# Kernel optimization log

Measured on AMD Instinct MI355X. Metric: run time of the kernel, lower is better.

## Reference

```python
import jax, jax.numpy as jnp
import numpy as np

EPS = 1e-5

def setup_inputs() -> dict:
    key = jax.random.key(0)
    k1, k2, k3, k4, k5 = jax.random.split(key, 5)
    B, N, K, HW, C = 2, 128, 64, 65536, 134
    # class probabilities (rows need not be normalized for the matcher math)
    input_class_prob = jax.random.uniform(k1, (B, N, C), dtype=jnp.float32)
    # predicted mask probabilities in [0, 1]
    input_mask = jax.random.uniform(k2, (B, N, HW), dtype=jnp.float32)
    # binary ground-truth masks (stored as float32 for the reduction math)
    target_mask = (jax.random.uniform(k3, (B, K, HW)) > 0.7).astype(jnp.float32)
    target_class = jax.random.randint(k4, (B, K), 0, C, dtype=jnp.int64)
    target_sizes = jax.random.randint(k5, (B,), 1, K + 1, dtype=jnp.int64)
    return {
        "input_class_prob": input_class_prob,
        "input_mask": input_mask,
        "target_mask": target_mask,
        "target_class": target_class,
        "target_sizes": target_sizes,
    }


def reference(input_class_prob, input_mask, target_mask, target_class, target_sizes):
    """Similarity-matrix stage of HungarianMatcher.

    Returns sim: (B, N, K) = sim_class * sim_dice.
    The subsequent scipy linear_sum_assignment is CPU-only with
    data-dependent shapes and is excluded from the kernelizable math.
    """
    B, N, _ = input_class_prob.shape
    K = target_class.shape[-1]
    # sim_class[b, n, k] = input_class_prob[b, n, target_class[b, k]]
    idx = jnp.broadcast_to(target_class[:, None, :], (B, N, K))
    sim_class = jnp.take_along_axis(input_class_prob, idx, axis=-1)
    # dice similarity without materializing the (B, N, K, HW) broadcast:
    # intersections via GEMM, cardinalities via row/col sums + broadcast.
    intersections = jnp.einsum("bnp,bkp->bnk", input_mask, target_mask)
    cardinalities = input_mask.sum(-1)[:, :, None] + target_mask.sum(-1)[:, None, :]
    sim_dice = (2.0 * intersections + EPS) / (cardinalities + EPS)
    return sim_class * sim_dice
```

## Files before the change

kernel.cpp:

```cpp
#include <hip/hip_runtime.h>

#define HWX 65536
#define NQ 128
#define KT 64
#define CC 134
#define BB 2
#define NW 128
#define WIN 512
#define SUB 128
#define NSUB 4
#define EPSI 1e-5f

typedef __attribute__((ext_vector_type(4))) float f32x4;
typedef __attribute__((ext_vector_type(8))) short bf16x8;
typedef __attribute__((ext_vector_type(4))) unsigned int u32x4;

static __device__ __forceinline__ unsigned int cvtpk(float lo, float hi) {
  unsigned int r;
  asm("v_cvt_pk_bf16_f32 %0, %1, %2" : "=v"(r) : "v"(lo), "v"(hi));
  return r;
}

__global__ void hm_detect(const unsigned int* __restrict__ t,
                          unsigned int* __restrict__ flag) {
  unsigned int w = t[threadIdx.x * 2 + 1];
  unsigned long long any = __ballot(w != 0u);
  if (threadIdx.x == 0) *flag = (any != 0ull) ? 1u : 0u;
}

template <bool ATOMIC>
__global__ __launch_bounds__(512)
void hm_stage1(const float* __restrict__ in_mask, const float* __restrict__ tg_mask,
               float* __restrict__ Ipart, float* __restrict__ RSin,
               float* __restrict__ RStg) {
  const int w = blockIdx.x & (NW - 1);
  const int b = blockIdx.x >> 7;
  const int tid = threadIdx.x;
  const int lane = tid & 63;
  const int wv = tid >> 6;
  const int srow = tid >> 4;
  const int scolb = (tid & 15) * 16;
  const int l16 = lane & 15;
  const int lg = lane >> 4;

  __shared__ unsigned short lA[2][128 * 128];
  __shared__ unsigned short lB[2][64 * 128];

  const float* Ab = in_mask + (size_t)b * NQ * HWX + (size_t)w * WIN;
  const float* Bb = tg_mask + (size_t)b * KT * HWX + (size_t)w * WIN;

  f32x4 la[8], lb[4];
  f32x4 acc[4];
  #pragma unroll
  for (int i = 0; i < 4; ++i) acc[i] = f32x4{0.f, 0.f, 0.f, 0.f};
  float rsA[4] = {0.f, 0.f, 0.f, 0.f};
  float rsB[2] = {0.f, 0.f};

  auto ISSUE = [&](int t) {
    #pragma unroll
    for (int it = 0; it < 4; ++it) {
      const float* p = Ab + (size_t)(it * 32 + srow) * HWX + t * SUB + (tid & 15) * 8;
      la[it * 2]     = *(const f32x4*)p;
      la[it * 2 + 1] = *(const f32x4*)(p + 4);
    }
    #pragma unroll
    for (int it = 0; it < 2; ++it) {
      const float* p = Bb + (size_t)(it * 32 + srow) * HWX + t * SUB + (tid & 15) * 8;
      lb[it * 2]     = *(const f32x4*)p;
      lb[it * 2 + 1] = *(const f32x4*)(p + 4);
    }
  };

  auto CVTW = [&](int buf) {
    char* A8 = (char*)lA[buf];
    char* B8 = (char*)lB[buf];
    #pragma unroll
    for (int it = 0; it < 4; ++it) {
      f32x4 x = la[it * 2], y = la[it * 2 + 1];
      rsA[it] += (x.x + x.y) + (x.z + x.w) + (y.x + y.y) + (y.z + y.w);
      u32x4 v;
      v.x = cvtpk(x.x, x.y); v.y = cvtpk(x.z, x.w);
      v.z = cvtpk(y.x, y.y); v.w = cvtpk(y.z, y.w);
      const int row = it * 32 + srow;
      *(u32x4*)(A8 + ((row * 256 + scolb) ^ ((row & 7) << 4))) = v;
    }
    #pragma unroll
    for (int it = 0; it < 2; ++it) {
      f32x4 x = lb[it * 2], y = lb[it * 2 + 1];
      rsB[it] += (x.x + x.y) + (x.z + x.w) + (y.x + y.y) + (y.z + y.w);
      u32x4 v;
      v.x = cvtpk(x.x, x.y); v.y = cvtpk(x.z, x.w);
      v.z = cvtpk(y.x, y.y); v.w = cvtpk(y.z, y.w);
      const int row = it * 32 + srow;
      *(u32x4*)(B8 + ((row * 256 + scolb) ^ ((row & 7) << 4))) = v;
    }
  };

  auto COMP = [&](int buf) {
    const char* A8 = (const char*)lA[buf];
    const char* B8 = (const char*)lB[buf];
    const int arow = wv * 16 + l16;
    const int sw = (l16 & 7) << 4;
    #pragma unroll
    for (int s = 0; s < 4; ++s) {
      bf16x8 fa = *(const bf16x8*)(A8 + ((arow * 256 + s * 64 + lg * 16) ^ sw));
      #pragma unroll
      for (int cf = 0; cf < 4; ++cf) {
        const int brow = cf * 16 + l16;
        bf16x8 fb = *(const bf16x8*)(B8 + ((brow * 256 + s * 64 + lg * 16) ^ sw));
        acc[cf] = __builtin_amdgcn_mfma_f32_16x16x32_bf16(fa, fb, acc[cf], 0, 0, 0);
      }
    }
  };

  ISSUE(0);
  CVTW(0);
  __syncthreads();
  #pragma unroll
  for (int t = 0; t < NSUB; ++t) {
    if (t + 1 < NSUB) ISSUE(t + 1);
    COMP(t & 1);
    if (t + 1 < NSUB) {
      CVTW((t + 1) & 1);
      __syncthreads();
    }
  }

  #pragma unroll
  for (int cf = 0; cf < 4; ++cf) {
    #pragma unroll
    for (int j = 0; j < 4; ++j) {
      const int row = wv * 16 + lg * 4 + j;
      const int col = cf * 16 + l16;
      if (!ATOMIC)
        Ipart[((size_t)(b * NW + w) * NQ + row) * KT + col] = acc[cf][j];
      else
        atomicAdd(&Ipart[((size_t)b * NQ + row) * KT + col], acc[cf][j]);
    }
  }

  #pragma unroll
  for (int it = 0; it < 4; ++it) {
    float v = rsA[it];
    v += __shfl_xor(v, 1); v += __shfl_xor(v, 2);
    v += __shfl_xor(v, 4); v += __shfl_xor(v, 8);
    rsA[it] = v;
  }
  #pragma unroll
  for (int it = 0; it < 2; ++it) {
    float v = rsB[it];
    v += __shfl_xor(v, 1); v += __shfl_xor(v, 2);
    v += __shfl_xor(v, 4); v += __shfl_xor(v, 8);
    rsB[it] = v;
  }
  if ((tid & 15) == 0) {
    if (!ATOMIC) {
      #pragma unroll
      for (int it = 0; it < 4; ++it)
        RSin[(size_t)(b * NW + w) * NQ + it * 32 + srow] = rsA[it];
      #pragma unroll
      for (int it = 0; it < 2; ++it)
        RStg[(size_t)(b * NW + w) * KT + it * 32 + srow] = rsB[it];
    } else {
      #pragma unroll
      for (int it = 0; it < 4; ++it)
        atomicAdd(&RSin[b * NQ + it * 32 + srow], rsA[it]);
      #pragma unroll
      for (int it = 0; it < 2; ++it)
        atomicAdd(&RStg[b * KT + it * 32 + srow], rsB[it]);
    }
  }
}

__global__ __launch_bounds__(256)
void hm_stage2(const float* __restrict__ cprob, const void* __restrict__ tcls,
               const float* __restrict__ Ipart, const float* __restrict__ RSin,
               const float* __restrict__ RStg, float* __restrict__ out) {
  const int bn = blockIdx.x;
  const int b = bn >> 7, n = bn & 127;
  const int k = threadIdx.x & 63;
  const int wq = threadIdx.x >> 6;
  float I = 0.f, ra = 0.f, rg = 0.f;
  #pragma unroll 4
  for (int ww = 0; ww < NW / 4; ++ww) {
    const int w = wq * (NW / 4) + ww;
    I  += Ipart[((size_t)(b * NW + w) * NQ + n) * KT + k];
    ra += RSin[(size_t)(b * NW + w) * NQ + n];
    rg += RStg[(size_t)(b * NW + w) * KT + k];
  }
  __shared__ float sI[4][64];
  __shared__ float sG[4][64];
  __shared__ float sR[4];
  sI[wq][k] = I;
  sG[wq][k] = rg;
  if (k == 0) sR[wq] = ra;
  __syncthreads();
  if (wq == 0) {
    I  = sI[0][k] + sI[1][k] + sI[2][k] + sI[3][k];
    rg = sG[0][k] + sG[1][k] + sG[2][k] + sG[3][k];
    ra = sR[0] + sR[1] + sR[2] + sR[3];
    const unsigned int hi = ((const unsigned int*)tcls)[k * 2 + 1];
    const bool i32 = (__ballot(hi != 0u) != 0ull);
    int tc = i32 ? ((const int*)tcls)[b * KT + k]
                 : (int)((const long long*)tcls)[b * KT + k];
    const float c = cprob[((size_t)b * NQ + n) * CC + tc];
    out[(size_t)bn * KT + k] = c * (2.f * I + EPSI) / (ra + rg + EPSI);
  }
}

__global__ __launch_bounds__(256)
void hm_stage2_direct(const float* __restrict__ cprob, const void* __restrict__ tcls,
                      const unsigned int* __restrict__ flag,
                      const float* __restrict__ Iacc, const float* __restrict__ RSin,
                      const float* __restrict__ RStg, float* __restrict__ out) {
  const int idx = blockIdx.x * 256 + threadIdx.x;
  const int k = idx & 63;
  const int n = (idx >> 6) & 127;
  const int b = idx >> 13;
  const float I  = Iacc[idx];
  const float ra = RSin[b * NQ + n];
  const float rg = RStg[b * KT + k];
  int tc;
  if (*flag) tc = ((const int*)tcls)[b * KT + k];
  else       tc = (int)((const long long*)tcls)[b * KT + k];
  const float c = cprob[((size_t)b * NQ + n) * CC + tc];
  out[idx] = c * (2.f * I + EPSI) / (ra + rg + EPSI);
}

__global__ void hm_zero(float* __restrict__ p, int n) {
  int i = blockIdx.x * blockDim.x + threadIdx.x;
  if (i < n) p[i] = 0.f;
}

extern "C" void kernel_launch(void* const* d_in, const int* in_sizes, int n_in,
                              void* d_out, int out_size, void* d_ws, size_t ws_size,
                              hipStream_t stream) {
  const float* cprob = (const float*)d_in[0];
  const float* imask = (const float*)d_in[1];
  const float* tmask = (const float*)d_in[2];
  const void*  tcls  = d_in[3];
  float* out = (float*)d_out;

  const size_t ipart_f = (size_t)BB * NW * NQ * KT;
  const size_t rsin_f  = (size_t)BB * NW * NQ;
  const size_t rstg_f  = (size_t)BB * NW * KT;
  const size_t need    = (ipart_f + rsin_f + rstg_f) * sizeof(float);

  char* ws = (char*)d_ws;
  if (ws_size >= need) {
    float* Ipart = (float*)ws;
    float* RSin  = Ipart + ipart_f;
    float* RStg  = RSin + rsin_f;
    hm_stage1<false><<<BB * NW, 512, 0, stream>>>(imask, tmask, Ipart, RSin, RStg);
    hm_stage2<<<BB * NQ, 256, 0, stream>>>(cprob, tcls, Ipart, RSin, RStg, out);
  } else {
    float* Iacc = (float*)ws;
    float* RSin = Iacc + (size_t)BB * NQ * KT;
    float* RStg = RSin + BB * NQ;
    unsigned int* flag = (unsigned int*)(RStg + BB * KT);
    const int zn = BB * NQ * KT + BB * NQ + BB * KT;
    hm_zero<<<(zn + 255) / 256, 256, 0, stream>>>(Iacc, zn);
    hm_detect<<<1, 64, 0, stream>>>((const unsigned int*)tcls, flag);
    hm_stage1<true><<<BB * NW, 512, 0, stream>>>(imask, tmask, Iacc, RSin, RStg);
    hm_stage2_direct<<<(BB * NQ * KT) / 256, 256, 0, stream>>>(cprob, tcls, flag, Iacc, RSin, RStg, out);
  }
}
```

Baseline: 27.58 us.

## Double-buffer register prefetch two subtiles ahead with LDS-only barriers

Adds a second register staging buffer so global loads for subtiles t+1 and t+2 are in flight while the current subtile is converted and run through MFMA. The loop is fully unrolled into an explicit schedule. `__syncthreads` is replaced by a barrier that waits only on LDS counters (lgkmcnt), so outstanding global loads are not drained at each barrier. The goal is better hiding of HBM latency in this bandwidth-bound GEMM stage. The cost is higher VGPR pressure from the extra staging registers, which could limit occupancy.

```diff
diff --git a/kernel.cpp b/kernel.cpp
--- a/kernel.cpp
+++ b/kernel.cpp
@@ -20,6 +20,12 @@
   asm("v_cvt_pk_bf16_f32 %0, %1, %2" : "=v"(r) : "v"(lo), "v"(hi));
   return r;
 }
+
+#define BAR()                                                \
+  do {                                                       \
+    asm volatile("s_waitcnt lgkmcnt(0)" ::: "memory");       \
+    __builtin_amdgcn_s_barrier();                            \
+  } while (0)
 
 __global__ void hm_detect(const unsigned int* __restrict__ t,
                           unsigned int* __restrict__ flag) {
@@ -49,34 +55,36 @@
   const float* Ab = in_mask + (size_t)b * NQ * HWX + (size_t)w * WIN;
   const float* Bb = tg_mask + (size_t)b * KT * HWX + (size_t)w * WIN;
 
-  f32x4 la[8], lb[4];
+  struct RS { f32x4 a[8]; f32x4 b[4]; };
+  RS r0, r1;
+
   f32x4 acc[4];
   #pragma unroll
   for (int i = 0; i < 4; ++i) acc[i] = f32x4{0.f, 0.f, 0.f, 0.f};
   float rsA[4] = {0.f, 0.f, 0.f, 0.f};
   float rsB[2] = {0.f, 0.f};
 
-  auto ISSUE = [&](int t) {
+  auto ISSUE = [&](RS& r, int t) {
     #pragma unroll
     for (int it = 0; it < 4; ++it) {
       const float* p = Ab + (size_t)(it * 32 + srow) * HWX + t * SUB + (tid & 15) * 8;
-      la[it * 2]     = *(const f32x4*)p;
-      la[it * 2 + 1] = *(const f32x4*)(p + 4);
+      r.a[it * 2]     = *(const f32x4*)p;
+      r.a[it * 2 + 1] = *(const f32x4*)(p + 4);
     }
     #pragma unroll
     for (int it = 0; it < 2; ++it) {
       const float* p = Bb + (size_t)(it * 32 + srow) * HWX + t * SUB + (tid & 15) * 8;
-      lb[it * 2]     = *(const f32x4*)p;
-      lb[it * 2 + 1] = *(const f32x4*)(p + 4);
+      r.b[it * 2]     = *(const f32x4*)p;
+      r.b[it * 2 + 1] = *(const f32x4*)(p + 4);
     }
   };
 
-  auto CVTW = [&](int buf) {
+  auto CVTW = [&](RS& r, int buf) {
     char* A8 = (char*)lA[buf];
     char* B8 = (char*)lB[buf];
     #pragma unroll
     for (int it = 0; it < 4; ++it) {
-      f32x4 x = la[it * 2], y = la[it * 2 + 1];
+      f32x4 x = r.a[it * 2], y = r.a[it * 2 + 1];
       rsA[it] += (x.x + x.y) + (x.z + x.w) + (y.x + y.y) + (y.z + y.w);
       u32x4 v;
       v.x = cvtpk(x.x, x.y); v.y = cvtpk(x.z, x.w);
@@ -86,7 +94,7 @@
     }
     #pragma unroll
     for (int it = 0; it < 2; ++it) {
-      f32x4 x = lb[it * 2], y = lb[it * 2 + 1];
+      f32x4 x = r.b[it * 2], y = r.b[it * 2 + 1];
       rsB[it] += (x.x + x.y) + (x.z + x.w) + (y.x + y.y) + (y.z + y.w);
       u32x4 v;
       v.x = cvtpk(x.x, x.y); v.y = cvtpk(x.z, x.w);
@@ -113,18 +121,22 @@
     }
   };
 
-  ISSUE(0);
-  CVTW(0);
-  __syncthreads();
-  #pragma unroll
-  for (int t = 0; t < NSUB; ++t) {
-    if (t + 1 < NSUB) ISSUE(t + 1);
-    COMP(t & 1);
-    if (t + 1 < NSUB) {
-      CVTW((t + 1) & 1);
-      __syncthreads();
-    }
-  }
+  ISSUE(r0, 0);
+  ISSUE(r1, 1);
+  CVTW(r0, 0);
+  BAR();
+  ISSUE(r0, 2);
+  COMP(0);
+  CVTW(r1, 1);
+  BAR();
+  ISSUE(r1, 3);
+  COMP(1);
+  CVTW(r0, 0);
+  BAR();
+  COMP(0);
+  CVTW(r1, 1);
+  BAR();
+  COMP(1);
 
   #pragma unroll
   for (int cf = 0; cf < 4; ++cf) {
```

Measured after the change: 27.88 us. About the same (+1.1%).
